# Performance work log

Measured on AMD Instinct MI355X. Metric: run time of the kernel, lower is better.

The kernel has to match this reference:

```python
import jax, jax.numpy as jnp
import numpy as np

C, B, N, IN, OUT = 32, 32, 4096, 16, 32
NUM_ITERS = 3


def _squash(t, axis=-1):
    # scale = |t|^2 / (1 + |t|^2); out = scale * t / |t|
    sn = jnp.sum(t * t, axis=axis, keepdims=True)
    return (sn / (1.0 + sn)) * t / jnp.sqrt(sn)


def setup_inputs() -> dict:
    key = jax.random.key(0)
    k1, k2 = jax.random.split(key)
    x = jax.random.normal(k1, (B, N, IN), dtype=jnp.float32)
    route_weights = jax.random.normal(k2, (C, N, IN, OUT), dtype=jnp.float32)
    return {"x": x, "route_weights": route_weights}


def reference(x, route_weights):
    # priors[c,b,n,d] = sum_i x[b,n,i] * W[c,n,i,d]  (torch: [C,B,N,1,D], singleton dropped)
    priors = jnp.einsum('bni,cnio->cbno', x, route_weights)  # [C,B,N,D]
    # torch logits are [C,B,N,1,D] but constant over D (delta broadcasts), and the
    # custom softmax normalizes over dim=2 (route nodes N), so [C,B,N] is equivalent.
    logits = jnp.zeros(priors.shape[:3], dtype=priors.dtype)  # [C,B,N]
    outputs = None
    for i in range(NUM_ITERS):
        probs = jax.nn.softmax(logits, axis=2)  # softmax over route nodes (dim=2)
        s = jnp.sum(probs[..., None] * priors, axis=2, keepdims=True)  # [C,B,1,D]
        outputs = _squash(s, axis=-1)
        if i != NUM_ITERS - 1:
            logits = logits + jnp.sum(priors * outputs, axis=-1)  # agreement [C,B,N]
    return outputs[:, :, :, None, :]  # [C,B,1,1,D] to match torch output shape
```

## Files before the change

### kernel.cpp

```cpp
#include <hip/hip_runtime.h>
#include <math.h>


typedef _Float16 f16x8 __attribute__((ext_vector_type(8)));
typedef float f32x16 __attribute__((ext_vector_type(16)));

namespace {
constexpr int kC = 32, kB = 32, kN = 4096, kI = 16, kD = 32;
constexpr int CHUNKS = 32;
constexpr int CHUNK_N = kN / CHUNKS;
constexpr int PS = kB * kD + kB;
constexpr int GRID = kC * CHUNKS;
constexpr size_t XT_ELEMS = (size_t)kN * kB * kI;
constexpr size_t P_FLOATS = (size_t)kC * CHUNKS * PS;
constexpr size_t CV_FLOATS = (size_t)kC * kB * kD;
constexpr size_t WS_BYTES = XT_ELEMS * 2 + (P_FLOATS + CV_FLOATS) * 4;
}

__device__ __forceinline__ f32x16 zero16() {
  f32x16 z;
#pragma unroll
  for (int r = 0; r < 16; ++r) z[r] = 0.f;
  return z;
}

__global__ __launch_bounds__(256) void k_xt(const float* __restrict__ x,
                                            _Float16* __restrict__ xt) {
  const int t = blockIdx.x * 256 + threadIdx.x;
  const int r = t >> 1, half = t & 1;
  const int b = r >> 12, n = r & 4095;
  const float4* s4 =
      reinterpret_cast<const float4*>(x) + (size_t)r * 4 + half * 2;
  const float4 f0 = s4[0], f1 = s4[1];
  f16x8 o;
  o[0] = (_Float16)f0.x; o[1] = (_Float16)f0.y;
  o[2] = (_Float16)f0.z; o[3] = (_Float16)f0.w;
  o[4] = (_Float16)f1.x; o[5] = (_Float16)f1.y;
  o[6] = (_Float16)f1.z; o[7] = (_Float16)f1.w;
  *reinterpret_cast<f16x8*>(xt + ((size_t)n * kB + b) * kI + half * 8) = o;
}

template <int MODE>
__global__ __launch_bounds__(256) void k_sweep(const float* __restrict__ W,
                                               const _Float16* __restrict__ xt,
                                               const float* __restrict__ cumVec,
                                               float* __restrict__ partials) {
  __shared__ float red[4][32][33];
  __shared__ float lred[4][32];
  const int bid = blockIdx.x;
  const int c = bid & 31;
  const int chunk = bid >> 5;
  const int tid = threadIdx.x;
  const int w = tid >> 6, l = tid & 63;
  const int m = l & 31, h = l >> 5;
  const int n0 = chunk * CHUNK_N;
  constexpr int TILES = CHUNK_N / 4;

  const float* wp = W + ((size_t)c * kN + n0 + w) * 512 + (h * 8) * 32 + m;
  const _Float16* xp = xt + ((size_t)(n0 + w)) * 512 + m * 16 + h * 8;

  float cvr[16];
  if (MODE) {
    const float* cvp = cumVec + (size_t)c * 1024 + m * 32;
#pragma unroll
    for (int r = 0; r < 16; ++r) cvr[r] = cvp[(r & 3) + 8 * (r >> 2) + 4 * h];
  }

  f32x16 accA = zero16(), accB = zero16();
  float lacc = 0.f;
  const f32x16 z = zero16();

  float rA0[8], rA1[8];
  f16x8 B0, B1;
#pragma unroll
  for (int j = 0; j < 8; ++j) rA0[j] = wp[j * 32];
  B0 = *reinterpret_cast<const f16x8*>(xp);
#pragma unroll
  for (int j = 0; j < 8; ++j) rA1[j] = wp[2048 + j * 32];
  B1 = *reinterpret_cast<const f16x8*>(xp + 2048);

#pragma unroll 1
  for (int t = 0; t < TILES; t += 2) {
    {
      f16x8 a;
#pragma unroll
      for (int j = 0; j < 8; ++j) a[j] = (_Float16)rA0[j];
      const f16x8 b = B0;
      const int tn = (t + 2 < TILES) ? t + 2 : 0;
#pragma unroll
      for (int j = 0; j < 8; ++j) rA0[j] = wp[(size_t)tn * 2048 + j * 32];
      B0 = *reinterpret_cast<const f16x8*>(xp + (size_t)tn * 2048);
      if constexpr (MODE == 0) {
        accA = __builtin_amdgcn_mfma_f32_32x32x16_f16(a, b, accA, 0, 0, 0);
      } else {
        const f32x16 pr =
            __builtin_amdgcn_mfma_f32_32x32x16_f16(a, b, z, 0, 0, 0);
        float d0 = pr[0] * cvr[0], d1 = pr[1] * cvr[1];
        float d2 = pr[2] * cvr[2], d3 = pr[3] * cvr[3];
#pragma unroll
        for (int r = 4; r < 16; r += 4) {
          d0 = fmaf(pr[r + 0], cvr[r + 0], d0);
          d1 = fmaf(pr[r + 1], cvr[r + 1], d1);
          d2 = fmaf(pr[r + 2], cvr[r + 2], d2);
          d3 = fmaf(pr[r + 3], cvr[r + 3], d3);
        }
        float dp = (d0 + d1) + (d2 + d3);
        dp += __shfl_xor(dp, 32);
        const float e = __expf(dp);
        lacc += e;
#pragma unroll
        for (int r = 0; r < 16; ++r) accA[r] = fmaf(e, pr[r], accA[r]);
      }
    }
    {
      f16x8 a;
#pragma unroll
      for (int j = 0; j < 8; ++j) a[j] = (_Float16)rA1[j];
      const f16x8 b = B1;
      const int tn = (t + 3 < TILES) ? t + 3 : 0;
#pragma unroll
      for (int j = 0; j < 8; ++j) rA1[j] = wp[(size_t)tn * 2048 + j * 32];
      B1 = *reinterpret_cast<const f16x8*>(xp + (size_t)tn * 2048);
      if constexpr (MODE == 0) {
        accB = __builtin_amdgcn_mfma_f32_32x32x16_f16(a, b, accB, 0, 0, 0);
      } else {
        const f32x16 pr =
            __builtin_amdgcn_mfma_f32_32x32x16_f16(a, b, z, 0, 0, 0);
        float d0 = pr[0] * cvr[0], d1 = pr[1] * cvr[1];
        float d2 = pr[2] * cvr[2], d3 = pr[3] * cvr[3];
#pragma unroll
        for (int r = 4; r < 16; r += 4) {
          d0 = fmaf(pr[r + 0], cvr[r + 0], d0);
          d1 = fmaf(pr[r + 1], cvr[r + 1], d1);
          d2 = fmaf(pr[r + 2], cvr[r + 2], d2);
          d3 = fmaf(pr[r + 3], cvr[r + 3], d3);
        }
        float dp = (d0 + d1) + (d2 + d3);
        dp += __shfl_xor(dp, 32);
        const float e = __expf(dp);
        lacc += e;
#pragma unroll
        for (int r = 0; r < 16; ++r) accB[r] = fmaf(e, pr[r], accB[r]);
      }
    }
  }
#pragma unroll
  for (int r = 0; r < 16; ++r) accA[r] += accB[r];

#pragma unroll
  for (int r = 0; r < 16; ++r)
    red[w][(r & 3) + 8 * (r >> 2) + 4 * h][m] = accA[r];
  if (MODE && h == 0) lred[w][m] = lacc;
  __syncthreads();

  float* Pp = partials + ((size_t)c * CHUNKS + chunk) * PS;
#pragma unroll
  for (int e = tid; e < 1024; e += 256) {
    const int d = e >> 5, bb = e & 31;
    Pp[e] = red[0][d][bb] + red[1][d][bb] + red[2][d][bb] + red[3][d][bb];
  }
  if (MODE && tid < 32)
    Pp[1024 + tid] = lred[0][tid] + lred[1][tid] + lred[2][tid] + lred[3][tid];
}

template <int K>
__global__ __launch_bounds__(1024) void k_reduce(
    const float* __restrict__ partials, float* __restrict__ CV,
    float* __restrict__ out) {
  const int c = blockIdx.x;
  const int t = threadIdx.x;
  const int b = t >> 5, d = t & 31;
  const float* Pc = partials + (size_t)c * CHUNKS * PS;
  float s = 0.f;
#pragma unroll 4
  for (int ch = 0; ch < CHUNKS; ++ch) s += Pc[(size_t)ch * PS + d * 32 + b];
  float inv;
  if constexpr (K == 0) {
    inv = 1.0f / (float)kN;
  } else {
    float lb = 0.f;
#pragma unroll 4
    for (int ch = 0; ch < CHUNKS; ++ch) lb += Pc[(size_t)ch * PS + 1024 + b];
    inv = 1.0f / lb;
  }
  const float sv = s * inv;
  float sn = sv * sv;
  sn += __shfl_xor(sn, 1);
  sn += __shfl_xor(sn, 2);
  sn += __shfl_xor(sn, 4);
  sn += __shfl_xor(sn, 8);
  sn += __shfl_xor(sn, 16);
  const float coef = sqrtf(sn) / (1.0f + sn);
  const float o = sv * coef;
  if constexpr (K == 2)
    out[(size_t)c * 1024 + t] = o;
  else if constexpr (K == 0)
    CV[(size_t)c * 1024 + t] = o;
  else
    CV[(size_t)c * 1024 + t] += o;
}

namespace v1 {
constexpr int BG = 4, NSLOT = 128, THREADS1 = NSLOT * 8;
template <int MODE>
__device__ __forceinline__ void sweep_pass(const float* __restrict__ Wc,
                                           const float* __restrict__ x, int b0,
                                           int tid, int nslot, int dg,
                                           float (*red)[8][20], float (*sS)[kD],
                                           float* sL, const float (*sVec)[kD]) {
  float acc[BG][4];
  float lv[BG];
#pragma unroll
  for (int b = 0; b < BG; ++b) {
    lv[b] = 0.f;
#pragma unroll
    for (int j = 0; j < 4; ++j) acc[b][j] = 0.f;
  }
  float vec[BG][4];
  if (MODE) {
#pragma unroll
    for (int b = 0; b < BG; ++b)
#pragma unroll
      for (int j = 0; j < 4; ++j) vec[b][j] = sVec[b][4 * dg + j];
  }
#pragma unroll 1
  for (int n = nslot; n < kN; n += NSLOT) {
    const float* Wn = Wc + (size_t)n * (kI * kD) + 4 * dg;
    float pr[BG][4];
#pragma unroll
    for (int b = 0; b < BG; ++b)
#pragma unroll
      for (int j = 0; j < 4; ++j) pr[b][j] = 0.f;
#pragma unroll
    for (int iq = 0; iq < 4; ++iq) {
      float4 wv[4];
#pragma unroll
      for (int r = 0; r < 4; ++r)
        wv[r] = *reinterpret_cast<const float4*>(Wn + (4 * iq + r) * kD);
#pragma unroll
      for (int b = 0; b < BG; ++b) {
        const float4 xv = *reinterpret_cast<const float4*>(
            x + ((size_t)(b0 + b) * kN + n) * kI + 4 * iq);
        const float xsv[4] = {xv.x, xv.y, xv.z, xv.w};
#pragma unroll
        for (int r = 0; r < 4; ++r) {
          pr[b][0] = fmaf(xsv[r], wv[r].x, pr[b][0]);
          pr[b][1] = fmaf(xsv[r], wv[r].y, pr[b][1]);
          pr[b][2] = fmaf(xsv[r], wv[r].z, pr[b][2]);
          pr[b][3] = fmaf(xsv[r], wv[r].w, pr[b][3]);
        }
      }
    }
    if (MODE == 0) {
#pragma unroll
      for (int b = 0; b < BG; ++b)
#pragma unroll
        for (int j = 0; j < 4; ++j) acc[b][j] += pr[b][j];
    } else {
#pragma unroll
      for (int b = 0; b < BG; ++b) {
        float dp = pr[b][0] * vec[b][0] + pr[b][1] * vec[b][1] +
                   pr[b][2] * vec[b][2] + pr[b][3] * vec[b][3];
        dp += __shfl_xor(dp, 1);
        dp += __shfl_xor(dp, 2);
        dp += __shfl_xor(dp, 4);
        const float e = __expf(dp);
        lv[b] += e;
        acc[b][0] = fmaf(e, pr[b][0], acc[b][0]);
        acc[b][1] = fmaf(e, pr[b][1], acc[b][1]);
        acc[b][2] = fmaf(e, pr[b][2], acc[b][2]);
        acc[b][3] = fmaf(e, pr[b][3], acc[b][3]);
      }
    }
  }
#pragma unroll
  for (int b = 0; b < BG; ++b) {
#pragma unroll
    for (int j = 0; j < 4; ++j) {
      float v = acc[b][j];
      v += __shfl_xor(v, 8);
      v += __shfl_xor(v, 16);
      v += __shfl_xor(v, 32);
      acc[b][j] = v;
    }
    if (MODE) {
      float v = lv[b];
      v += __shfl_xor(v, 8);
      v += __shfl_xor(v, 16);
      v += __shfl_xor(v, 32);
      lv[b] = v;
    }
  }
  const int lane = tid & 63;
  const int wv_id = tid >> 6;
  if ((lane >> 3) == 0) {
#pragma unroll
    for (int b = 0; b < BG; ++b) {
#pragma unroll
      for (int j = 0; j < 4; ++j) red[wv_id][dg][4 * b + j] = acc[b][j];
      if (MODE) red[wv_id][dg][16 + b] = lv[b];
    }
  }
  __syncthreads();
  if (tid < 128) {
    const int dgc = tid >> 4, e = tid & 15;
    float s = 0.f;
#pragma unroll
    for (int w = 0; w < 16; ++w) s += red[w][dgc][e];
    sS[e >> 2][4 * dgc + (e & 3)] = s;
  }
  if (MODE && tid >= 128 && tid < 128 + BG) {
    const int b = tid - 128;
    float s = 0.f;
#pragma unroll
    for (int w = 0; w < 16; ++w) s += red[w][0][16 + b];
    sL[b] = s;
  }
  __syncthreads();
}

__global__ __launch_bounds__(THREADS1, 4) void caps_route_kernel(
    const float* __restrict__ x, const float* __restrict__ W,
    float* __restrict__ out) {
  __shared__ float red[16][8][20];
  __shared__ float sS[BG][kD];
  __shared__ float sVec[BG][kD];
  __shared__ float sL[BG];
  const int i = blockIdx.x;
  const int xcd = i & 7;
  const int j = i >> 3;
  const int c = xcd + 8 * (j >> 3);
  const int b0 = 4 * (j & 7);
  const int tid = threadIdx.x;
  const int nslot = tid >> 3;
  const int dg = tid & 7;
  const float* Wc = W + (size_t)c * kN * kI * kD;
  sweep_pass<0>(Wc, x, b0, tid, nslot, dg, red, sS, sL, sVec);
  if (tid < BG) {
    const int b = tid;
    float sval[kD], sn = 0.f;
    const float inv = 1.0f / (float)kN;
#pragma unroll
    for (int d = 0; d < kD; ++d) {
      sval[d] = sS[b][d] * inv;
      sn += sval[d] * sval[d];
    }
    const float coef = sqrtf(sn) / (1.0f + sn);
#pragma unroll
    for (int d = 0; d < kD; ++d) sVec[b][d] = sval[d] * coef;
  }
  __syncthreads();
  sweep_pass<1>(Wc, x, b0, tid, nslot, dg, red, sS, sL, sVec);
  if (tid < BG) {
    const int b = tid;
    float sval[kD], sn = 0.f;
    const float inv = 1.0f / sL[b];
#pragma unroll
    for (int d = 0; d < kD; ++d) {
      sval[d] = sS[b][d] * inv;
      sn += sval[d] * sval[d];
    }
    const float coef = sqrtf(sn) / (1.0f + sn);
#pragma unroll
    for (int d = 0; d < kD; ++d) sVec[b][d] += sval[d] * coef;
  }
  __syncthreads();
  sweep_pass<1>(Wc, x, b0, tid, nslot, dg, red, sS, sL, sVec);
  if (tid < BG) {
    const int b = tid;
    float sval[kD], sn = 0.f;
    const float inv = 1.0f / sL[b];
#pragma unroll
    for (int d = 0; d < kD; ++d) {
      sval[d] = sS[b][d] * inv;
      sn += sval[d] * sval[d];
    }
    const float coef = sqrtf(sn) / (1.0f + sn);
    float* o = out + ((size_t)c * kB + (b0 + b)) * kD;
#pragma unroll
    for (int d = 0; d < kD; ++d) o[d] = sval[d] * coef;
  }
}
}

extern "C" void kernel_launch(void* const* d_in, const int* in_sizes, int n_in,
                              void* d_out, int out_size, void* d_ws,
                              size_t ws_size, hipStream_t stream) {
  const float* x = (const float*)d_in[0];
  const float* W = (const float*)d_in[1];
  float* out = (float*)d_out;
  (void)in_sizes; (void)n_in; (void)out_size;

  if (ws_size < WS_BYTES) {
    v1::caps_route_kernel<<<256, v1::THREADS1, 0, stream>>>(x, W, out);
    return;
  }
  _Float16* xt = (_Float16*)d_ws;
  float* P = (float*)(xt + XT_ELEMS);
  float* CV = P + P_FLOATS;

  k_xt<<<GRID, 256, 0, stream>>>(x, xt);
  k_sweep<0><<<GRID, 256, 0, stream>>>(W, xt, nullptr, P);
  k_reduce<0><<<kC, 1024, 0, stream>>>(P, CV, nullptr);
  k_sweep<1><<<GRID, 256, 0, stream>>>(W, xt, CV, P);
  k_reduce<1><<<kC, 1024, 0, stream>>>(P, CV, nullptr);
  k_sweep<1><<<GRID, 256, 0, stream>>>(W, xt, CV, P);
  k_reduce<2><<<kC, 1024, 0, stream>>>(P, nullptr, out);
}
```

Baseline: 203.1 us.

## Cache fp16 copy of route weights in first sweep for later routing sweeps

When the workspace is large enough, the first sweep now writes a half-precision copy of the fp32 route weights alongside its normal work, reading the fp32 weights with nontemporal loads. The two later routing sweeps use a new kernel that reads this fp16 copy with vector loads instead of re-reading and converting the fp32 weights. This halves weight traffic in the later sweeps and drops their per-element conversions. The cost is an extra large write in the first sweep and a much larger workspace requirement. Without that workspace the code falls back to the previous path.

```diff
diff --git a/kernel.cpp b/kernel.cpp
--- a/kernel.cpp
+++ b/kernel.cpp
@@ -12,9 +12,12 @@
 constexpr int PS = kB * kD + kB;
 constexpr int GRID = kC * CHUNKS;
 constexpr size_t XT_ELEMS = (size_t)kN * kB * kI;
+constexpr size_t WT_ELEMS = (size_t)kC * kN * kI * kD;
 constexpr size_t P_FLOATS = (size_t)kC * CHUNKS * PS;
 constexpr size_t CV_FLOATS = (size_t)kC * kB * kD;
-constexpr size_t WS_BYTES = XT_ELEMS * 2 + (P_FLOATS + CV_FLOATS) * 4;
+constexpr size_t WS_BYTES_MID = XT_ELEMS * 2 + (P_FLOATS + CV_FLOATS) * 4;
+constexpr size_t WS_BYTES_BIG =
+    (XT_ELEMS + WT_ELEMS) * 2 + (P_FLOATS + CV_FLOATS) * 4;
 }
 
 __device__ __forceinline__ f32x16 zero16() {
@@ -40,11 +43,12 @@
   *reinterpret_cast<f16x8*>(xt + ((size_t)n * kB + b) * kI + half * 8) = o;
 }
 
-template <int MODE>
+template <int MODE, bool EMIT>
 __global__ __launch_bounds__(256) void k_sweep(const float* __restrict__ W,
                                                const _Float16* __restrict__ xt,
                                                const float* __restrict__ cumVec,
-                                               float* __restrict__ partials) {
+                                               float* __restrict__ partials,
+                                               _Float16* __restrict__ Wt) {
   __shared__ float red[4][32][33];
   __shared__ float lred[4][32];
   const int bid = blockIdx.x;
@@ -58,6 +62,8 @@
 
   const float* wp = W + ((size_t)c * kN + n0 + w) * 512 + (h * 8) * 32 + m;
   const _Float16* xp = xt + ((size_t)(n0 + w)) * 512 + m * 16 + h * 8;
+  _Float16* wtp =
+      EMIT ? (Wt + ((size_t)c * kN + n0 + w) * 512 + (size_t)l * 8) : nullptr;
 
   float cvr[16];
   if (MODE) {
@@ -73,10 +79,13 @@
   float rA0[8], rA1[8];
   f16x8 B0, B1;
 #pragma unroll
-  for (int j = 0; j < 8; ++j) rA0[j] = wp[j * 32];
+  for (int j = 0; j < 8; ++j)
+    rA0[j] = EMIT ? __builtin_nontemporal_load(wp + j * 32) : wp[j * 32];
   B0 = *reinterpret_cast<const f16x8*>(xp);
 #pragma unroll
-  for (int j = 0; j < 8; ++j) rA1[j] = wp[2048 + j * 32];
+  for (int j = 0; j < 8; ++j)
+    rA1[j] = EMIT ? __builtin_nontemporal_load(wp + 2048 + j * 32)
+                  : wp[2048 + j * 32];
   B1 = *reinterpret_cast<const f16x8*>(xp + 2048);
 
 #pragma unroll 1
@@ -88,8 +97,13 @@
       const f16x8 b = B0;
       const int tn = (t + 2 < TILES) ? t + 2 : 0;
 #pragma unroll
-      for (int j = 0; j < 8; ++j) rA0[j] = wp[(size_t)tn * 2048 + j * 32];
+      for (int j = 0; j < 8; ++j)
+        rA0[j] = EMIT ? __builtin_nontemporal_load(wp + (size_t)tn * 2048 +
+                                                   j * 32)
+                      : wp[(size_t)tn * 2048 + j * 32];
       B0 = *reinterpret_cast<const f16x8*>(xp + (size_t)tn * 2048);
+      if constexpr (EMIT)
+        *reinterpret_cast<f16x8*>(wtp + (size_t)t * 2048) = a;
       if constexpr (MODE == 0) {
         accA = __builtin_amdgcn_mfma_f32_32x32x16_f16(a, b, accA, 0, 0, 0);
       } else {
@@ -119,8 +133,13 @@
       const f16x8 b = B1;
       const int tn = (t + 3 < TILES) ? t + 3 : 0;
 #pragma unroll
-      for (int j = 0; j < 8; ++j) rA1[j] = wp[(size_t)tn * 2048 + j * 32];
+      for (int j = 0; j < 8; ++j)
+        rA1[j] = EMIT ? __builtin_nontemporal_load(wp + (size_t)tn * 2048 +
+                                                   j * 32)
+                      : wp[(size_t)tn * 2048 + j * 32];
       B1 = *reinterpret_cast<const f16x8*>(xp + (size_t)tn * 2048);
+      if constexpr (EMIT)
+        *reinterpret_cast<f16x8*>(wtp + (size_t)(t + 1) * 2048) = a;
       if constexpr (MODE == 0) {
         accB = __builtin_amdgcn_mfma_f32_32x32x16_f16(a, b, accB, 0, 0, 0);
       } else {
@@ -160,6 +179,108 @@
     Pp[e] = red[0][d][bb] + red[1][d][bb] + red[2][d][bb] + red[3][d][bb];
   }
   if (MODE && tid < 32)
+    Pp[1024 + tid] = lred[0][tid] + lred[1][tid] + lred[2][tid] + lred[3][tid];
+}
+
+__global__ __launch_bounds__(256) void k_sweep_wt(
+    const _Float16* __restrict__ Wt, const _Float16* __restrict__ xt,
+    const float* __restrict__ cumVec, float* __restrict__ partials) {
+  __shared__ float red[4][32][33];
+  __shared__ float lred[4][32];
+  const int bid = blockIdx.x;
+  const int c = bid & 31;
+  const int chunk = bid >> 5;
+  const int tid = threadIdx.x;
+  const int w = tid >> 6, l = tid & 63;
+  const int m = l & 31, h = l >> 5;
+  const int n0 = chunk * CHUNK_N;
+  constexpr int TILES = CHUNK_N / 4;
+
+  const _Float16* wp = Wt + ((size_t)c * kN + n0 + w) * 512 + (size_t)l * 8;
+  const _Float16* xp = xt + ((size_t)(n0 + w)) * 512 + m * 16 + h * 8;
+
+  float cvr[16];
+  const float* cvp = cumVec + (size_t)c * 1024 + m * 32;
+#pragma unroll
+  for (int r = 0; r < 16; ++r) cvr[r] = cvp[(r & 3) + 8 * (r >> 2) + 4 * h];
+
+  f32x16 accA = zero16(), accB = zero16();
+  float lacc = 0.f;
+  const f32x16 z = zero16();
+
+  f16x8 A0, A1, B0, B1;
+  A0 = *reinterpret_cast<const f16x8*>(wp);
+  B0 = *reinterpret_cast<const f16x8*>(xp);
+  A1 = *reinterpret_cast<const f16x8*>(wp + 2048);
+  B1 = *reinterpret_cast<const f16x8*>(xp + 2048);
+
+#pragma unroll 1
+  for (int t = 0; t < TILES; t += 2) {
+    {
+      const f16x8 a = A0;
+      const f16x8 b = B0;
+      const int tn = (t + 2 < TILES) ? t + 2 : 0;
+      A0 = *reinterpret_cast<const f16x8*>(wp + (size_t)tn * 2048);
+      B0 = *reinterpret_cast<const f16x8*>(xp + (size_t)tn * 2048);
+      const f32x16 pr =
+          __builtin_amdgcn_mfma_f32_32x32x16_f16(a, b, z, 0, 0, 0);
+      float d0 = pr[0] * cvr[0], d1 = pr[1] * cvr[1];
+      float d2 = pr[2] * cvr[2], d3 = pr[3] * cvr[3];
+#pragma unroll
+      for (int r = 4; r < 16; r += 4) {
+        d0 = fmaf(pr[r + 0], cvr[r + 0], d0);
+        d1 = fmaf(pr[r + 1], cvr[r + 1], d1);
+        d2 = fmaf(pr[r + 2], cvr[r + 2], d2);
+        d3 = fmaf(pr[r + 3], cvr[r + 3], d3);
+      }
+      float dp = (d0 + d1) + (d2 + d3);
+      dp += __shfl_xor(dp, 32);
+      const float e = __expf(dp);
+      lacc += e;
+#pragma unroll
+      for (int r = 0; r < 16; ++r) accA[r] = fmaf(e, pr[r], accA[r]);
+    }
+    {
+      const f16x8 a = A1;
+      const f16x8 b = B1;
+      const int tn = (t + 3 < TILES) ? t + 3 : 0;
+      A1 = *reinterpret_cast<const f16x8*>(wp + (size_t)tn * 2048);
+      B1 = *reinterpret_cast<const f16x8*>(xp + (size_t)tn * 2048);
+      const f32x16 pr =
+          __builtin_amdgcn_mfma_f32_32x32x16_f16(a, b, z, 0, 0, 0);
+      float d0 = pr[0] * cvr[0], d1 = pr[1] * cvr[1];
+      float d2 = pr[2] * cvr[2], d3 = pr[3] * cvr[3];
+#pragma unroll
+      for (int r = 4; r < 16; r += 4) {
+        d0 = fmaf(pr[r + 0], cvr[r + 0], d0);
+        d1 = fmaf(pr[r + 1], cvr[r + 1], d1);
+        d2 = fmaf(pr[r + 2], cvr[r + 2], d2);
+        d3 = fmaf(pr[r + 3], cvr[r + 3], d3);
+      }
+      float dp = (d0 + d1) + (d2 + d3);
+      dp += __shfl_xor(dp, 32);
+      const float e = __expf(dp);
+      lacc += e;
+#pragma unroll
+      for (int r = 0; r < 16; ++r) accB[r] = fmaf(e, pr[r], accB[r]);
+    }
+  }
+#pragma unroll
+  for (int r = 0; r < 16; ++r) accA[r] += accB[r];
+
+#pragma unroll
+  for (int r = 0; r < 16; ++r)
+    red[w][(r & 3) + 8 * (r >> 2) + 4 * h][m] = accA[r];
+  if (h == 0) lred[w][m] = lacc;
+  __syncthreads();
+
+  float* Pp = partials + ((size_t)c * CHUNKS + chunk) * PS;
+#pragma unroll
+  for (int e = tid; e < 1024; e += 256) {
+    const int d = e >> 5, bb = e & 31;
+    Pp[e] = red[0][d][bb] + red[1][d][bb] + red[2][d][bb] + red[3][d][bb];
+  }
+  if (tid < 32)
     Pp[1024 + tid] = lred[0][tid] + lred[1][tid] + lred[2][tid] + lred[3][tid];
 }
 
@@ -391,19 +512,36 @@
   float* out = (float*)d_out;
   (void)in_sizes; (void)n_in; (void)out_size;
 
-  if (ws_size < WS_BYTES) {
-    v1::caps_route_kernel<<<256, v1::THREADS1, 0, stream>>>(x, W, out);
+  if (ws_size >= WS_BYTES_BIG) {
+    _Float16* xt = (_Float16*)d_ws;
+    _Float16* Wt = xt + XT_ELEMS;
+    float* P = (float*)(Wt + WT_ELEMS);
+    float* CV = P + P_FLOATS;
+
+    k_xt<<<GRID, 256, 0, stream>>>(x, xt);
+    k_sweep<0, true><<<GRID, 256, 0, stream>>>(W, xt, nullptr, P, Wt);
+    k_reduce<0><<<kC, 1024, 0, stream>>>(P, CV, nullptr);
+    k_sweep_wt<<<GRID, 256, 0, stream>>>(Wt, xt, CV, P);
+    k_reduce<1><<<kC, 1024, 0, stream>>>(P, CV, nullptr);
+    k_sweep_wt<<<GRID, 256, 0, stream>>>(Wt, xt, CV, P);
+    k_reduce<2><<<kC, 1024, 0, stream>>>(P, nullptr, out);
     return;
   }
-  _Float16* xt = (_Float16*)d_ws;
-  float* P = (float*)(xt + XT_ELEMS);
-  float* CV = P + P_FLOATS;
-
-  k_xt<<<GRID, 256, 0, stream>>>(x, xt);
-  k_sweep<0><<<GRID, 256, 0, stream>>>(W, xt, nullptr, P);
-  k_reduce<0><<<kC, 1024, 0, stream>>>(P, CV, nullptr);
-  k_sweep<1><<<GRID, 256, 0, stream>>>(W, xt, CV, P);
-  k_reduce<1><<<kC, 1024, 0, stream>>>(P, CV, nullptr);
-  k_sweep<1><<<GRID, 256, 0, stream>>>(W, xt, CV, P);
-  k_reduce<2><<<kC, 1024, 0, stream>>>(P, nullptr, out);
-}
+
+  if (ws_size >= WS_BYTES_MID) {
+    _Float16* xt = (_Float16*)d_ws;
+    float* P = (float*)(xt + XT_ELEMS);
+    float* CV = P + P_FLOATS;
+
+    k_xt<<<GRID, 256, 0, stream>>>(x, xt);
+    k_sweep<0, false><<<GRID, 256, 0, stream>>>(W, xt, nullptr, P, nullptr);
+    k_reduce<0><<<kC, 1024, 0, stream>>>(P, CV, nullptr);
+    k_sweep<1, false><<<GRID, 256, 0, stream>>>(W, xt, CV, P, nullptr);
+    k_reduce<1><<<kC, 1024, 0, stream>>>(P, CV, nullptr);
+    k_sweep<1, false><<<GRID, 256, 0, stream>>>(W, xt, CV, P, nullptr);
+    k_reduce<2><<<kC, 1024, 0, stream>>>(P, nullptr, out);
+    return;
+  }
+
+  v1::caps_route_kernel<<<256, v1::THREADS1, 0, stream>>>(x, W, out);
+}
```

After: 201.0 us. No clear change (-1.0%).
